# Performance work log

Measured on AMD Instinct MI355X. Metric: run time of the kernel, lower is better.

Reference implementation:

```python
import jax, jax.numpy as jnp
import numpy as np

BIG = 10000000.0

def heaviside(x):
    return (jnp.tanh(BIG * x) + 1.0) * 0.5

def interception(Prec, PET, INSC):
    INSC = jnp.clip(INSC * 5.0, 0.5, 5.0)
    IMAX = jnp.maximum(jnp.minimum(INSC, PET), 0.0)
    INT = jnp.maximum(jnp.minimum(IMAX, Prec), 0.0)
    INR = jnp.maximum(Prec - INT, 0.0)
    return INT, INR

def soil_moisture_store(SMS1, SMSC):
    SMSC = jnp.clip(SMSC * 500.0, 50.0, 500.0)
    return jnp.maximum(jnp.minimum(SMS1, SMSC), 0.0)

def soil_fluxes(PET, INT, INR, COEFF, SQ, SMSC, SUB, CRAK, SMS1):
    COEFF = jnp.clip(COEFF * 400.0, 50.0, 400.0)
    SQ = jnp.clip(SQ * 6.0, 0.0, 6.0)
    SMSC = jnp.clip(SMSC * 500.0, 50.0, 500.0)
    SUB = jnp.clip(SUB, 0.0, 1.0)
    CRAK = jnp.clip(CRAK, 0.0, 1.0)
    cap = COEFF * jnp.exp(-SQ * SMS1 / SMSC)
    RMO = jnp.maximum(heaviside(cap - INR) * INR + heaviside(INR - cap) * cap, 0.0)
    IRUN = jnp.maximum(INR - RMO, 0.0)
    SRUN = jnp.maximum(SUB * (SMS1 / SMSC) * RMO, 0.0)
    REC = jnp.maximum(CRAK * (SMS1 / SMSC) * (RMO - SRUN), 0.0)
    SMF = jnp.maximum(RMO - SRUN - REC, 0.0)
    POT = jnp.maximum(PET - INT, 0.0)
    r = 10.0 * SMS1 / SMSC
    ETS = jnp.maximum(heaviside(r - POT) * POT + heaviside(POT - r) * r, 0.0)
    return RMO, IRUN, SRUN, REC, SMF, ETS

def recharge_calculation(SMS1, SMSC, REC, SMF, ETS):
    SMSC = jnp.clip(SMSC * 500.0, 50.0, 500.0)
    s = SMS1 + SMF - ETS
    RECnew = heaviside(s - SMSC) * (REC + s - SMSC) + heaviside(SMSC - s) * REC
    return jnp.maximum(RECnew, 0.0)

def groundwaterstore(GW1, RecK):
    RecK = jnp.clip(RecK * 0.3, 0.003, 0.3)
    return jnp.maximum(heaviside(GW1) * (RecK * GW1), 0.0)

def _forward(inputs, INSC, COEFF, SQ, SMSC, SUB, CRAK, RecK):
    B, T, _ = inputs.shape
    xs = jnp.transpose(inputs, (1, 0, 2))  # (T, B, 2)

    def step(carry, x):
        SMS1, GW1 = carry  # each (B, 1)
        Prec, PET = x[:, 0:1], x[:, 1:2]
        INT, INR = interception(Prec, PET, INSC)
        SMS1c = soil_moisture_store(SMS1, SMSC)
        RMO, IRUN, SRUN, REC, SMF, ETS = soil_fluxes(PET, INT, INR, COEFF, SQ, SMSC, SUB, CRAK, SMS1c)
        next_SMS = SMS1c + jnp.clip(SMF - ETS, -100000.0, 100000.0)
        RECnew = recharge_calculation(SMS1c, SMSC, REC, SMF, ETS)
        BAS = groundwaterstore(GW1, RecK)
        next_GW = GW1 + jnp.clip(RECnew - BAS, -100000.0, 100000.0)
        return (next_SMS, next_GW), jnp.concatenate([next_SMS, next_GW], axis=1)

    init = (jnp.zeros((B, 1), inputs.dtype), jnp.zeros((B, 1), inputs.dtype))
    _, outs = jax.lax.scan(step, init, xs)  # (T, B, 2)
    outs = jnp.transpose(outs, (1, 0, 2))   # (B, T, 2)
    outs = jnp.roll(outs, shift=1, axis=1)  # state at step t-1 (wrap like tf.roll)
    SMS1 = outs[:, :, 0:1]
    GW1 = outs[:, :, 1:2]
    Prec = inputs[:, :, 0:1]
    PET = inputs[:, :, 1:2]
    INT, INR = interception(Prec, PET, INSC)
    SMS1 = soil_moisture_store(SMS1, SMSC)
    RMO, IRUN, SRUN, REC, SMF, ETS = soil_fluxes(PET, INT, INR, COEFF, SQ, SMSC, SUB, CRAK, SMS1)
    RECnew = recharge_calculation(SMS1, SMSC, REC, SMF, ETS)
    BAS = groundwaterstore(GW1, RecK)
    DR = jnp.maximum(SRUN + IRUN, 0.0)
    GD = jnp.maximum(BAS, 0.0)
    Q = jnp.maximum(DR + GD, 0.0)
    return Q  # (B, T, 1)


def setup_inputs() -> dict:
    key = jax.random.key(0)
    k1, = jax.random.split(key, 1)
    B, T = 4096, 1024
    # Prec in [0, 20) mm/day, PET in [0, 8) mm/day
    u = jax.random.uniform(k1, (B, T, 2), dtype=jnp.float32)
    scale = jnp.array([20.0, 8.0], dtype=jnp.float32)
    inputs = u * scale
    p = lambda v: jnp.full((1,), v, dtype=jnp.float32)
    return {
        "inputs": inputs,
        "INSC": p(0.5), "COEFF": p(0.5), "SQ": p(0.5), "SMSC": p(0.5),
        "SUB": p(0.5), "CRAK": p(0.5), "RecK": p(0.5),
    }


def reference(inputs, INSC, COEFF, SQ, SMSC, SUB, CRAK, RecK):
    return _forward(inputs, INSC, COEFF, SQ, SMSC, SUB, CRAK, RecK)
```

## Files before the change

### kernel.cpp

```cpp
#include <hip/hip_runtime.h>
#include <hip/hip_bf16.h>
#include <math.h>


struct P {
    float INSC, SMSC, RecK, g1, lc, k1, k2, k3, c2;
};

__device__ __forceinline__ P make_params(const float* pINSC, const float* pCOEFF,
                                         const float* pSQ,   const float* pSMSC,
                                         const float* pSUB,  const float* pCRAK,
                                         const float* pRecK) {
    P p;
    p.INSC      = fminf(fmaxf(pINSC[0]  * 5.0f,   0.5f),   5.0f);
    float COEFF = fminf(fmaxf(pCOEFF[0] * 400.0f, 50.0f),  400.0f);
    float SQ    = fminf(fmaxf(pSQ[0]    * 6.0f,   0.0f),   6.0f);
    p.SMSC      = fminf(fmaxf(pSMSC[0]  * 500.0f, 50.0f),  500.0f);
    float SUB   = fminf(fmaxf(pSUB[0],  0.0f), 1.0f);
    float CRAK  = fminf(fmaxf(pCRAK[0], 0.0f), 1.0f);
    p.RecK      = fminf(fmaxf(pRecK[0]  * 0.3f,   0.003f), 0.3f);
    p.g1 = 1.0f - p.RecK;
    p.lc = log2f(COEFF);
    float inv = 1.0f / p.SMSC;
    p.k1 = SUB * inv;
    p.k2 = CRAK * inv;
    p.k3 = 10.0f * inv;
    p.c2 = (-SQ * inv) * 1.44269504088896340736f;
    return p;
}

__device__ __forceinline__ float step(float Prec, float PET, float& sms, float& gw, const P& p) {
    float INT  = fminf(fminf(p.INSC, PET), Prec);
    float INR  = Prec - INT;
    float POT  = PET - INT;
    float S    = fminf(sms, p.SMSC);
    float u    = fmaf(-p.k1, S, 1.0f);
    float v    = fmaf(-p.k2, S, 1.0f);
    float ETS  = fminf(POT, p.k3 * S);
    float SmE  = S - ETS;
    float e    = exp2f(fmaf(p.c2, S, p.lc));
    float RMO  = fminf(INR, e);
    float w    = u * RMO;
    float s2   = fmaf(v, w, SmE);
    float SMF  = v * w;
    float REC  = w - SMF;
    float RECnew = REC + fmaxf(s2 - p.SMSC, 0.0f);
    float BAS  = p.RecK * gw;
    float Q    = (INR - w) + BAS;
    gw  = fmaf(p.g1, gw, RECnew);
    sms = s2;
    return Q;
}

__device__ __forceinline__ void stepw(float Prec, float PET, float& sms, float& gw, const P& p) {
    float INT  = fminf(fminf(p.INSC, PET), Prec);
    float INR  = Prec - INT;
    float POT  = PET - INT;
    float S    = fminf(sms, p.SMSC);
    float u    = fmaf(-p.k1, S, 1.0f);
    float v    = fmaf(-p.k2, S, 1.0f);
    float ETS  = fminf(POT, p.k3 * S);
    float SmE  = S - ETS;
    float e    = exp2f(fmaf(p.c2, S, p.lc));
    float RMO  = fminf(INR, e);
    float w    = u * RMO;
    float s2   = fmaf(v, w, SmE);
    float SMF  = v * w;
    float REC  = w - SMF;
    float RECnew = REC + fmaxf(s2 - p.SMSC, 0.0f);
    gw  = fmaf(p.g1, gw, RECnew);
    sms = s2;
}

__device__ __forceinline__ void dstep(float Prec, float PET,
                                      float& slo, float& shi, float& gw, const P& p) {
    float INT = fminf(fminf(p.INSC, PET), Prec);
    float INR = Prec - INT;
    float POT = PET - INT;
    {
        float S    = fminf(shi, p.SMSC);
        float u    = fmaf(-p.k1, S, 1.0f);
        float v    = fmaf(-p.k2, S, 1.0f);
        float ETS  = fminf(POT, p.k3 * S);
        float SmE  = S - ETS;
        float e    = exp2f(fmaf(p.c2, S, p.lc));
        float RMO  = fminf(INR, e);
        float w    = u * RMO;
        float s2   = fmaf(v, w, SmE);
        float SMF  = v * w;
        float REC  = w - SMF;
        float RECnew = REC + fmaxf(s2 - p.SMSC, 0.0f);
        gw  = fmaf(p.g1, gw, RECnew);
        shi = s2;
    }
    {
        float S    = fminf(slo, p.SMSC);
        float u    = fmaf(-p.k1, S, 1.0f);
        float v    = fmaf(-p.k2, S, 1.0f);
        float ETS  = fminf(POT, p.k3 * S);
        float SmE  = S - ETS;
        float e    = exp2f(fmaf(p.c2, S, p.lc));
        float RMO  = fminf(INR, e);
        float w    = u * RMO;
        slo = fmaf(v, w, SmE);
    }
}

#define MERGE_TOL 0.75f


#define LB(DST, K, NB) do { int _kn = (K) < (NB) ? (K) : (NB) - 1;              \
    _Pragma("unroll") for (int _q = 0; _q < 4; ++_q) DST[_q] = bp[4 * _kn + _q]; } while (0)

#define PIPE3(NB, CB) do { if ((NB) > 0) {                                      \
    LB(B0, 0, (NB)); LB(B1, 1, (NB));                                           \
    int _j = 0;                                                                 \
    for (; _j + 3 <= (NB); _j += 3) {                                           \
        LB(B2, _j + 2, (NB)); CB(B0, _j);                                       \
        LB(B0, _j + 3, (NB)); CB(B1, _j + 1);                                   \
        LB(B1, _j + 4, (NB)); CB(B2, _j + 2);                                   \
    }                                                                           \
    if (_j < (NB)) { LB(B2, _j + 2, (NB)); CB(B0, _j); ++_j;                    \
        if (_j < (NB)) { LB(B0, _j + 2, (NB)); CB(B1, _j); } }                  \
} } while (0)

#define CBW(BUF, J) do { _Pragma("unroll") for (int _m = 0; _m < 4; ++_m) {     \
    stepw(BUF[_m].x, BUF[_m].y, shi, gw, p);                                    \
    stepw(BUF[_m].z, BUF[_m].w, shi, gw, p); } } while (0)

#define CBD(BUF, J) do { _Pragma("unroll") for (int _m = 0; _m < 4; ++_m) {     \
    dstep(BUF[_m].x, BUF[_m].y, slo, shi, gw, p);                               \
    dstep(BUF[_m].z, BUF[_m].w, slo, shi, gw, p); } } while (0)

#define CBM(BUF, J) do { int _tb = 8 * (J);                                     \
    _Pragma("unroll") for (int _m = 0; _m < 4; ++_m) {                          \
    float _qa = step(BUF[_m].x, BUF[_m].y, sms, gw, p);                         \
    float _qb = step(BUF[_m].z, BUF[_m].w, sms, gw, p);                         \
    lds_q[_tb + 2 * _m][l] = _qa; lds_q[_tb + 2 * _m + 1][l] = _qb; } } while (0)

#define CBF(BUF, J) do { _Pragma("unroll") for (int _m = 0; _m < 4; ++_m) {     \
    float _qa = step(BUF[_m].x, BUF[_m].y, sms, gw, p);                         \
    float _qb = step(BUF[_m].z, BUF[_m].w, sms, gw, p);                         \
    orow2[ib0 + 4 * (J) + _m] = make_float2(_qa, _qb); } } while (0)


template<int T, int NC, int W>
__global__ __launch_bounds__(64, 1)
void hir_pass1(const float* __restrict__ inputs,
               const float* __restrict__ pINSC,  const float* __restrict__ pCOEFF,
               const float* __restrict__ pSQ,    const float* __restrict__ pSMSC,
               const float* __restrict__ pSUB,   const float* __restrict__ pCRAK,
               const float* __restrict__ pRecK,
               float* __restrict__ out, float4* __restrict__ st, int B)
{
    __shared__ float lds_q[64][65];
    const int l   = threadIdx.x;
    const int gid = blockIdx.x * 64 + l;
    const int b = gid % B;
    const int c = gid / B;
    if (c >= NC) return;

    P p = make_params(pINSC, pCOEFF, pSQ, pSMSC, pSUB, pCRAK, pRecK);

    const float4* __restrict__ rp = (const float4*)(inputs + (size_t)b * (2 * T));
    float* __restrict__ orow = out + (size_t)b * T;

    constexpr int CH = T / NC;
    const int i1 = (c * CH) >> 1;
    int i0 = i1 - (W >> 1);
    const bool exact = (i0 <= 0);
    if (i0 < 0) i0 = 0;

    float slo = 0.0f, shi = exact ? 0.0f : p.SMSC, gw = 0.0f;
    float4 B0[4], B1[4], B2[4];

    {
        const int nb = (i1 - i0) >> 2;
        const float4* bp = rp + i0;
        if (exact) {
            PIPE3(nb, CBW);
            slo = shi;
        } else {
            PIPE3(nb, CBD);
        }
    }
    const bool merged = exact || ((shi - slo) <= MERGE_TOL);
    float sms = exact ? shi : (0.5f * (slo + shi));

    {
        const float4* bp = rp + i1;
        PIPE3(8, CBM);
    }

    st[(size_t)c * B + b] = make_float4(sms, gw, merged ? 1.0f : 0.0f, 0.0f);

    float q0 = 0.0f;
    const bool hasq0 = (c == NC - 1);
    if (hasq0) {
        float4 f0 = rp[0];
        float ss = sms, gg = gw;
        q0 = step(f0.x, f0.y, ss, gg, p);
    }

    __syncthreads();

    const int b0 = b - l;
    const int t1 = c * CH;
    if (c == 0) {
        if (l > 0) {
            for (int j = 0; j < 64; ++j)
                out[(size_t)(b0 + j) * T + l] = lds_q[l][j];
        }
    } else {
        for (int j = 0; j < 64; ++j)
            out[(size_t)(b0 + j) * T + t1 + l] = lds_q[l][j];
    }
    if (hasq0) orow[0] = q0;
}


template<int T, int NC>
__global__ __launch_bounds__(64)
void hir_fixup(const float* __restrict__ inputs,
               const float* __restrict__ pINSC,  const float* __restrict__ pCOEFF,
               const float* __restrict__ pSQ,    const float* __restrict__ pSMSC,
               const float* __restrict__ pSUB,   const float* __restrict__ pCRAK,
               const float* __restrict__ pRecK,
               float* __restrict__ out, const float4* __restrict__ st, int B)
{
    const int gid = blockIdx.x * 64 + threadIdx.x;
    const int b = gid % B;
    const int c = gid / B;
    if (c >= NC) return;

    float4 sc = st[(size_t)c * B + b];
    if (sc.z != 0.0f) return;

    P p = make_params(pINSC, pCOEFF, pSQ, pSMSC, pSUB, pCRAK, pRecK);
    constexpr int CH = T / NC;

    const float4* __restrict__ rp = (const float4*)(inputs + (size_t)b * (2 * T));
    float* __restrict__ orow = out + (size_t)b * T;
    float2* __restrict__ orow2 = (float2*)orow;

    int m = c - 1;
    float4 sm = st[(size_t)m * B + b];
    while (sm.z == 0.0f) { --m; sm = st[(size_t)m * B + b]; }
    float sms = sm.x, gw = sm.y;

    float4 B0[4], B1[4], B2[4];

    {
        const int ia = ((m + 1) * CH) >> 1;
        const int ibx = (c * CH) >> 1;
        const int nb = (ibx - ia) >> 2;
        const float4* bp = rp + ia;
        float& shi = sms;
        PIPE3(nb, CBW);
    }

    {
        const int ib0 = (c * CH) >> 1;
        const float4* bp = rp + ib0;
        PIPE3(8, CBF);
    }

    if (c == NC - 1) {
        float4 f0 = rp[0];
        float ss = sms, gg = gw;
        orow[0] = step(f0.x, f0.y, ss, gg, p);
    }
}

template<int T>
__global__ __launch_bounds__(64, 1)
void hir_scan_kernel(const float* __restrict__ inputs,
                     const float* __restrict__ pINSC,  const float* __restrict__ pCOEFF,
                     const float* __restrict__ pSQ,    const float* __restrict__ pSMSC,
                     const float* __restrict__ pSUB,   const float* __restrict__ pCRAK,
                     const float* __restrict__ pRecK,
                     float* __restrict__ out, int B)
{
    int b = blockIdx.x * blockDim.x + threadIdx.x;
    if (b >= B) return;
    P p = make_params(pINSC, pCOEFF, pSQ, pSMSC, pSUB, pCRAK, pRecK);
    const float4* __restrict__ rp = (const float4*)(inputs + (size_t)b * (2 * T));
    float* __restrict__ orow = out + (size_t)b * T;
    float sms = 0.0f, gw = 0.0f;
    float4 cur = rp[0];
    const float P0 = cur.x, E0 = cur.y;
    constexpr int NI = T / 2;
    for (int i = 0; i < NI; ++i) {
        int ni = (i + 1 < NI) ? (i + 1) : i;
        float4 nxt = rp[ni];
        float qa = step(cur.x, cur.y, sms, gw, p);
        float qb = step(cur.z, cur.w, sms, gw, p);
        if (i == 0) { orow[1] = qb; }
        else        { ((float2*)orow)[i] = make_float2(qa, qb); }
        cur = nxt;
    }
    float ss = sms, gg = gw;
    orow[0] = step(P0, E0, ss, gg, p);
}

extern "C" void kernel_launch(void* const* d_in, const int* in_sizes, int n_in,
                              void* d_out, int out_size, void* d_ws, size_t ws_size,
                              hipStream_t stream) {
    (void)n_in; (void)out_size;
    constexpr int T  = 1024;
    constexpr int NC = 16;
    constexpr int W  = 320;
    const float* inputs = (const float*)d_in[0];
    const float* INSC   = (const float*)d_in[1];
    const float* COEFF  = (const float*)d_in[2];
    const float* SQ     = (const float*)d_in[3];
    const float* SMSC   = (const float*)d_in[4];
    const float* SUB    = (const float*)d_in[5];
    const float* CRAK   = (const float*)d_in[6];
    const float* RecK   = (const float*)d_in[7];
    float* out = (float*)d_out;

    int B = in_sizes[0] / (2 * T);
    size_t stBytes = (size_t)B * NC * sizeof(float4);

    if ((B % 64) == 0 && ws_size >= stBytes) {
        float4* st = (float4*)d_ws;
        long total = (long)B * NC;
        int blocks = (int)((total + 63) / 64);
        hir_pass1<T, NC, W><<<dim3(blocks), dim3(64), 0, stream>>>(
            inputs, INSC, COEFF, SQ, SMSC, SUB, CRAK, RecK, out, st, B);
        hir_fixup<T, NC><<<dim3(blocks), dim3(64), 0, stream>>>(
            inputs, INSC, COEFF, SQ, SMSC, SUB, CRAK, RecK, out, st, B);
        return;
    }

    int blocks = (B + 63) / 64;
    hir_scan_kernel<T><<<dim3(blocks), dim3(64), 0, stream>>>(
        inputs, INSC, COEFF, SQ, SMSC, SUB, CRAK, RecK, out, B);
}
```

Baseline: 117.6 us.

## Split dual-bound warm-up scan across two wavefronts per pass1 block

```diff
diff --git a/kernel.cpp b/kernel.cpp
--- a/kernel.cpp
+++ b/kernel.cpp
@@ -145,7 +145,7 @@
 
 
 template<int T, int NC, int W>
-__global__ __launch_bounds__(64, 1)
+__global__ __launch_bounds__(128, 1)
 void hir_pass1(const float* __restrict__ inputs,
                const float* __restrict__ pINSC,  const float* __restrict__ pCOEFF,
                const float* __restrict__ pSQ,    const float* __restrict__ pSMSC,
@@ -154,11 +154,14 @@
                float* __restrict__ out, float4* __restrict__ st, int B)
 {
     __shared__ float lds_q[64][65];
-    const int l   = threadIdx.x;
-    const int gid = blockIdx.x * 64 + l;
-    const int b = gid % B;
-    const int c = gid / B;
-    if (c >= NC) return;
+    __shared__ float lds_slo[64];
+    const int tid = threadIdx.x;
+    const int l = tid & 63;
+    const int w = tid >> 6;
+    const int nbg = B >> 6;
+    const int g = blockIdx.x % nbg;
+    const int c = blockIdx.x / nbg;
+    const int b = (g << 6) + l;
 
     P p = make_params(pINSC, pCOEFF, pSQ, pSMSC, pSUB, pCRAK, pRecK);
 
@@ -171,51 +174,57 @@
     const bool exact = (i0 <= 0);
     if (i0 < 0) i0 = 0;
 
-    float slo = 0.0f, shi = exact ? 0.0f : p.SMSC, gw = 0.0f;
+    float s  = exact ? 0.0f : (w ? 0.0f : p.SMSC);
+    float gw = 0.0f;
     float4 B0[4], B1[4], B2[4];
 
-    {
+    if (w == 0 || !exact) {
         const int nb = (i1 - i0) >> 2;
         const float4* bp = rp + i0;
-        if (exact) {
-            PIPE3(nb, CBW);
-            slo = shi;
-        } else {
-            PIPE3(nb, CBD);
-        }
-    }
-    const bool merged = exact || ((shi - slo) <= MERGE_TOL);
-    float sms = exact ? shi : (0.5f * (slo + shi));
-
-    {
-        const float4* bp = rp + i1;
-        PIPE3(8, CBM);
-    }
-
-    st[(size_t)c * B + b] = make_float4(sms, gw, merged ? 1.0f : 0.0f, 0.0f);
+        float& shi = s;
+        PIPE3(nb, CBW);
+    }
+
+    if (w) lds_slo[l] = s;
+    __syncthreads();
 
     float q0 = 0.0f;
     const bool hasq0 = (c == NC - 1);
-    if (hasq0) {
-        float4 f0 = rp[0];
-        float ss = sms, gg = gw;
-        q0 = step(f0.x, f0.y, ss, gg, p);
+    if (w == 0) {
+        const float slo = exact ? s : lds_slo[l];
+        const float shi = s;
+        const bool merged = exact || ((shi - slo) <= MERGE_TOL);
+        float sms = exact ? s : (0.5f * (slo + shi));
+
+        {
+            const float4* bp = rp + i1;
+            PIPE3(8, CBM);
+        }
+
+        st[(size_t)c * B + b] = make_float4(sms, gw, merged ? 1.0f : 0.0f, 0.0f);
+
+        if (hasq0) {
+            float4 f0 = rp[0];
+            float ss = sms, gg = gw;
+            q0 = step(f0.x, f0.y, ss, gg, p);
+        }
     }
 
     __syncthreads();
 
-    const int b0 = b - l;
+    const int b0 = g << 6;
     const int t1 = c * CH;
+    const int j0 = w << 5;
     if (c == 0) {
         if (l > 0) {
-            for (int j = 0; j < 64; ++j)
+            for (int j = j0; j < j0 + 32; ++j)
                 out[(size_t)(b0 + j) * T + l] = lds_q[l][j];
         }
     } else {
-        for (int j = 0; j < 64; ++j)
+        for (int j = j0; j < j0 + 32; ++j)
             out[(size_t)(b0 + j) * T + t1 + l] = lds_q[l][j];
     }
-    if (hasq0) orow[0] = q0;
+    if (w == 0 && hasq0) orow[0] = q0;
 }
 
 
@@ -325,11 +334,12 @@
 
     if ((B % 64) == 0 && ws_size >= stBytes) {
         float4* st = (float4*)d_ws;
+        int blocksP = (B >> 6) * NC;
+        hir_pass1<T, NC, W><<<dim3(blocksP), dim3(128), 0, stream>>>(
+            inputs, INSC, COEFF, SQ, SMSC, SUB, CRAK, RecK, out, st, B);
         long total = (long)B * NC;
-        int blocks = (int)((total + 63) / 64);
-        hir_pass1<T, NC, W><<<dim3(blocks), dim3(64), 0, stream>>>(
-            inputs, INSC, COEFF, SQ, SMSC, SUB, CRAK, RecK, out, st, B);
-        hir_fixup<T, NC><<<dim3(blocks), dim3(64), 0, stream>>>(
+        int blocksF = (int)((total + 63) / 64);
+        hir_fixup<T, NC><<<dim3(blocksF), dim3(64), 0, stream>>>(
             inputs, INSC, COEFF, SQ, SMSC, SUB, CRAK, RecK, out, st, B);
         return;
     }
```

After: 125.5 us. +6.7%, slower.
